# Performance work log

Hardware: AMD Instinct MI355X
Metric: run time of the kernel (lower is better)

The kernel has to match this reference:

```python
import jax, jax.numpy as jnp
import numpy as np

WIN_SIZE = 16
STRIDE = 8
H = W = 512
B = 8
C = 3


def gaussian_blend(win_size):
    # matches WindowOverlapProcessor._create_gaussian_weights
    sigma = win_size / 4.0
    x = jnp.arange(win_size, dtype=jnp.float32) - (win_size - 1) / 2.0
    g = jnp.exp(-(x ** 2) / (2.0 * sigma ** 2))
    g = g / g.sum()
    return g[:, None] * g[None, :]  # [ws, ws]


def setup_inputs() -> dict:
    key = jax.random.key(0)
    hw = (H - WIN_SIZE) // STRIDE + 1  # 63
    ww = (W - WIN_SIZE) // STRIDE + 1  # 63
    nw = hw * ww  # 3969
    hs = (jnp.arange(hw) * STRIDE).astype(jnp.int64 if jax.config.jax_enable_x64 else jnp.int32)
    ws_ = (jnp.arange(ww) * STRIDE).astype(hs.dtype)
    coords = jnp.stack(
        [jnp.repeat(hs, ww), jnp.tile(ws_, hw)], axis=-1
    )  # [nw, 2] regular overlapping grid
    windows = jax.random.normal(key, (B, nw, WIN_SIZE, WIN_SIZE, C), dtype=jnp.float32)
    return {
        "windows": windows,
        "window_coords": coords,
        "h_windows": hw,
        "w_windows": ww,
        "stride": STRIDE,
        "original_h": H,
        "original_w": W,
        "channels": C,
    }


def reference(windows, window_coords, h_windows, w_windows, stride,
              original_h, original_w, channels):
    Bb, nw, ws, _, Cc = windows.shape
    blend = gaussian_blend(ws)  # [ws, ws]

    # flat pixel index for every window element
    dh = jnp.arange(ws)
    dw = jnp.arange(ws)
    offs = dh[:, None] * original_w + dw[None, :]            # [ws, ws]
    base = window_coords[:, 0] * original_w + window_coords[:, 1]  # [nw]
    idx = (base[:, None, None] + offs[None]).reshape(-1)     # [nw*ws*ws]

    # weighted window values, [B, C, nw*ws*ws]
    contrib = windows * blend[None, None, :, :, None]
    contrib = contrib.transpose(0, 4, 1, 2, 3).reshape(Bb, Cc, -1)

    recon = jnp.zeros((Bb, Cc, original_h * original_w), windows.dtype)
    recon = recon.at[:, :, idx].add(contrib)

    wsum = jnp.zeros((original_h * original_w,), blend.dtype)
    wsum = wsum.at[idx].add(jnp.tile(blend.reshape(-1), nw))

    recon = recon / (wsum[None, None, :] + 1e-8)
    return recon.reshape(Bb, Cc, original_h, original_w)
```

## Files before the change

kernel.cpp:

```cpp
#include <hip/hip_runtime.h>


#define OH 512
#define OW 512
#define NB 8
#define NC 3
#define WSZ 16
#define STR 8
#define HWIN 63
#define NWIN (63 * 63)

__global__ __launch_bounds__(256) void window_overlap_kernel(
    const float* __restrict__ win, float* __restrict__ out) {
    __shared__ float gs[16];
    const int tid = threadIdx.x;
    if (tid < 16) {
        float x = (float)tid - 7.5f;
        gs[tid] = expf(-(x * x) * (1.0f / 32.0f));
    }
    __syncthreads();
    if (tid == 0) {
        float s = 0.0f;
#pragma unroll
        for (int i = 0; i < 16; ++i) s += gs[i];
        float inv = 1.0f / s;
#pragma unroll
        for (int i = 0; i < 16; ++i) gs[i] *= inv;
    }
    __syncthreads();

    const int idx = blockIdx.x * 256 + tid;
    const int w = idx & (OW - 1);
    const int h = (idx >> 9) & (OH - 1);
    const int b = idx >> 18;

    const int ilo = max((h - 8) >> 3, 0);
    const int ihi = min(h >> 3, HWIN - 1);
    const int jlo = max((w - 8) >> 3, 0);
    const int jhi = min(w >> 3, HWIN - 1);

    float acc0 = 0.0f, acc1 = 0.0f, acc2 = 0.0f, wsum = 0.0f;
    for (int i = ilo; i <= ihi; ++i) {
        const int dh = h - i * STR;
        const float gh = gs[dh];
        const int rowbase = (b * NWIN + i * HWIN) * (WSZ * WSZ) + dh * WSZ;
        for (int j = jlo; j <= jhi; ++j) {
            const int dw = w - j * STR;
            const float g = gh * gs[dw];
            const int base = (rowbase + j * (WSZ * WSZ) + dw) * NC;
            acc0 += g * win[base + 0];
            acc1 += g * win[base + 1];
            acc2 += g * win[base + 2];
            wsum += g;
        }
    }

    const float r = 1.0f / (wsum + 1e-8f);
    const int p = h * OW + w;
    float* ob = out + (size_t)b * NC * (OH * OW);
    ob[p] = acc0 * r;
    ob[OH * OW + p] = acc1 * r;
    ob[2 * OH * OW + p] = acc2 * r;
}

extern "C" void kernel_launch(void* const* d_in, const int* in_sizes, int n_in,
                              void* d_out, int out_size, void* d_ws, size_t ws_size,
                              hipStream_t stream) {
    const float* windows = (const float*)d_in[0];
    float* out = (float*)d_out;
    const int total = NB * OH * OW;
    window_overlap_kernel<<<total / 256, 256, 0, stream>>>(windows, out);
}
```

Before: 163.9 us.

## Compute eight adjacent output pixels per thread with vectorized window loads

Each thread now produces an 8-pixel horizontal strip aligned to the stride, so all eight pixels share the same set of overlapping windows. The 24 contiguous floats per window row are read with six float4 loads, and the outputs are written as float4 stores. The weight sum is factored into a row sum times per-column sums. This reduces per-pixel index math and scalar loads, but it cuts the thread count by eight and raises register pressure from the 32 accumulators.

```diff
diff --git a/kernel.cpp b/kernel.cpp
--- a/kernel.cpp
+++ b/kernel.cpp
@@ -30,37 +30,66 @@
     __syncthreads();
 
     const int idx = blockIdx.x * 256 + tid;
-    const int w = idx & (OW - 1);
-    const int h = (idx >> 9) & (OH - 1);
-    const int b = idx >> 18;
+    const int tw = idx & 63;
+    const int h  = (idx >> 6) & (OH - 1);
+    const int b  = idx >> 15;
+    const int w0 = tw * STR;
 
     const int ilo = max((h - 8) >> 3, 0);
     const int ihi = min(h >> 3, HWIN - 1);
-    const int jlo = max((w - 8) >> 3, 0);
-    const int jhi = min(w >> 3, HWIN - 1);
+    const int jlo = max(tw - 1, 0);
+    const int jhi = min(tw, HWIN - 1);
 
-    float acc0 = 0.0f, acc1 = 0.0f, acc2 = 0.0f, wsum = 0.0f;
-    for (int i = ilo; i <= ihi; ++i) {
-        const int dh = h - i * STR;
-        const float gh = gs[dh];
-        const int rowbase = (b * NWIN + i * HWIN) * (WSZ * WSZ) + dh * WSZ;
-        for (int j = jlo; j <= jhi; ++j) {
-            const int dw = w - j * STR;
-            const float g = gh * gs[dw];
-            const int base = (rowbase + j * (WSZ * WSZ) + dw) * NC;
-            acc0 += g * win[base + 0];
-            acc1 += g * win[base + 1];
-            acc2 += g * win[base + 2];
-            wsum += g;
+    float acc0[8], acc1[8], acc2[8], wk[8];
+#pragma unroll
+    for (int k = 0; k < 8; ++k) { acc0[k] = acc1[k] = acc2[k] = wk[k] = 0.0f; }
+
+    float hsum = 0.0f;
+    for (int i = ilo; i <= ihi; ++i) hsum += gs[h - i * STR];
+
+    for (int j = jlo; j <= jhi; ++j) {
+        const int dw0 = (tw - j) * STR;
+        float gw[8];
+#pragma unroll
+        for (int k = 0; k < 8; ++k) { gw[k] = gs[dw0 + k]; wk[k] += gw[k]; }
+
+        for (int i = ilo; i <= ihi; ++i) {
+            const int dh = h - i * STR;
+            const float gh = gs[dh];
+            const float* p = win +
+                (size_t)(((b * NWIN + i * HWIN + j) * (WSZ * WSZ) + dh * WSZ + dw0) * NC);
+            float vals[24];
+            const float4* p4 = (const float4*)p;
+            float4* v4 = (float4*)vals;
+            v4[0] = p4[0]; v4[1] = p4[1]; v4[2] = p4[2];
+            v4[3] = p4[3]; v4[4] = p4[4]; v4[5] = p4[5];
+#pragma unroll
+            for (int k = 0; k < 8; ++k) {
+                const float g = gh * gw[k];
+                acc0[k] += g * vals[k * 3 + 0];
+                acc1[k] += g * vals[k * 3 + 1];
+                acc2[k] += g * vals[k * 3 + 2];
+            }
         }
     }
 
-    const float r = 1.0f / (wsum + 1e-8f);
-    const int p = h * OW + w;
-    float* ob = out + (size_t)b * NC * (OH * OW);
-    ob[p] = acc0 * r;
-    ob[OH * OW + p] = acc1 * r;
-    ob[2 * OH * OW + p] = acc2 * r;
+    float r[8];
+#pragma unroll
+    for (int k = 0; k < 8; ++k) r[k] = 1.0f / (hsum * wk[k] + 1e-8f);
+
+    float* ob = out + (size_t)b * NC * (OH * OW) + h * OW + w0;
+    {
+        float4 o;
+        float4* q = (float4*)ob;
+        o = make_float4(acc0[0]*r[0], acc0[1]*r[1], acc0[2]*r[2], acc0[3]*r[3]); q[0] = o;
+        o = make_float4(acc0[4]*r[4], acc0[5]*r[5], acc0[6]*r[6], acc0[7]*r[7]); q[1] = o;
+        q = (float4*)(ob + OH * OW);
+        o = make_float4(acc1[0]*r[0], acc1[1]*r[1], acc1[2]*r[2], acc1[3]*r[3]); q[0] = o;
+        o = make_float4(acc1[4]*r[4], acc1[5]*r[5], acc1[6]*r[6], acc1[7]*r[7]); q[1] = o;
+        q = (float4*)(ob + 2 * OH * OW);
+        o = make_float4(acc2[0]*r[0], acc2[1]*r[1], acc2[2]*r[2], acc2[3]*r[3]); q[0] = o;
+        o = make_float4(acc2[4]*r[4], acc2[5]*r[5], acc2[6]*r[6], acc2[7]*r[7]); q[1] = o;
+    }
 }
 
 extern "C" void kernel_launch(void* const* d_in, const int* in_sizes, int n_in,
@@ -68,6 +97,6 @@
                               hipStream_t stream) {
     const float* windows = (const float*)d_in[0];
     float* out = (float*)d_out;
-    const int total = NB * OH * OW;
+    const int total = NB * OH * (OW / STR);
     window_overlap_kernel<<<total / 256, 256, 0, stream>>>(windows, out);
 }
```

Measured after the change: 167.7 us. 1.02x slower.
